# Optimization experiments

Measured on AMD Instinct MI355X. Metric: run time of the kernel, lower is better.

The kernel has to match this reference:

```python
import jax, jax.numpy as jnp
import numpy as np
from jax.scipy.special import erf

# synthetic covalent radii table (original imports `covalent_radii`, e.g. from ase)
COV_RADII = jnp.asarray(0.3 + 0.02 * np.arange(100), dtype=jnp.float32)

B_MOL = 1024   # molecules per batch
N_ATOM = 128   # atoms per molecule (equal-sized ragged batch, atoms sorted by molecule)
N_ELEM = 10


def setup_inputs() -> dict:
    key = jax.random.key(0)
    ks = jax.random.split(key, 6)
    N = B_MOL * N_ATOM
    return {
        "eneg": jax.random.normal(ks[0], (N, 1), jnp.float32),
        "positions": jax.random.normal(ks[1], (N, 3), jnp.float32) * 3.0,
        "node_attrs": jax.random.uniform(ks[2], (N, N_ELEM), jnp.float32),
        "hardness": jax.random.uniform(ks[3], (N_ELEM,), jnp.float32),
        "total_charge": jax.random.normal(ks[4], (B_MOL,), jnp.float32),
        "batch": jnp.repeat(jnp.arange(B_MOL), N_ATOM),          # sorted molecule ids
        "atomic_numbers": jax.random.randint(ks[5], (N,), 1, 90),
    }


def reference(eneg, positions, node_attrs, hardness, total_charge, batch, atomic_numbers):
    # atoms are sorted by molecule with equal molecule sizes, so the ragged
    # python loop of the original collapses to a batched [B, n, ...] computation.
    B = total_charge.shape[0]
    N = positions.shape[0]
    n = N // B
    sqrt_pi = jnp.sqrt(jnp.asarray(np.pi, jnp.float32))
    sqrt_2 = jnp.sqrt(jnp.asarray(2.0, jnp.float32))

    pos = positions.reshape(B, n, 3)
    Z = atomic_numbers.reshape(B, n)
    atom_idx = jnp.argmax(node_attrs, axis=1).reshape(B, n)

    r = COV_RADII[Z]                                     # [B, n]
    diag_vals = hardness[atom_idx] + 1.0 / (sqrt_pi * r)  # [B, n]
    sigma = jnp.square(r)                                # [B, n]
    gamma = jnp.sqrt(sigma[:, :, None] + sigma[:, None, :])  # [B, n, n]

    diff = pos[:, :, None, :] - pos[:, None, :, :]       # [B, n, n, 3]
    sq = jnp.sum(diff * diff, axis=-1)                   # [B, n, n]
    eye = jnp.eye(n, dtype=bool)
    dist = jnp.sqrt(jnp.where(eye, 1.0, sq))             # safe diag (overwritten below)

    A = erf(dist / (sqrt_2 * gamma)) / dist              # [B, n, n]
    A = jnp.where(eye, diag_vals[:, :, None], A)         # scatter hardness diagonal

    # augment with charge-conservation row/column of ones (corner = 1)
    A = jnp.concatenate([A, jnp.ones((B, n, 1), A.dtype)], axis=2)
    A = jnp.concatenate([A, jnp.ones((B, 1, n + 1), A.dtype)], axis=1)

    b = jnp.concatenate([-eneg.reshape(B, n, 1),
                         total_charge.reshape(B, 1, 1)], axis=1)  # [B, n+1, 1]

    x = jnp.linalg.solve(A, b)                           # batched small solves
    return x[:, :n, 0].reshape(-1)                       # partial charges, [N]
```

## Files before the change

kernel.cpp:

```cpp
#include <hip/hip_runtime.h>
#include <math.h>

#define NMOL  1024
#define N     128
#define NELEM 10
#define BLOCK 256
#define PW    8
#define NPAN  16
#define PSTR  12
#define USTR  132

typedef __attribute__((ext_vector_type(4))) float f4;


__global__ __launch_bounds__(BLOCK, 2) void ceq_solve_kernel(
    const float* __restrict__ eneg,
    const float* __restrict__ positions,
    const float* __restrict__ node_attrs,
    const float* __restrict__ hardness,
    const float* __restrict__ total_charge,
    const int*   __restrict__ atomic_numbers,
    float* __restrict__ out)
{
    __shared__ __align__(16) float P[2][2][N * PSTR];
    __shared__ __align__(16) float Up[2][PW * USTR];
    __shared__ __align__(16) float Ublk[2][NPAN][PW][PW];
    __shared__ float Dinv[2][PW], Dd[2][PW];
    __shared__ float rhsY[2][N], rhsZ[2][N];
    __shared__ float sxY[2][N], sxZ[2][N];
    __shared__ float px[2][N], py[2][N], pz[2][N], sg[2][N], dgv[2][N];
    __shared__ float lamS[2];

    const int tid  = threadIdx.x;
    const int lane = tid & 63;
    const int g    = tid >> 7;
    const int gt   = tid & 127;
    const int wv   = (tid >> 6) & 1;
    const int r0   = 2 * lane;
    const int r1   = r0 + 1;
    const int mol  = 2 * blockIdx.x + g;
    const int base = mol * N;

    {
        const int i = gt;
        const int Z = atomic_numbers[base + i];
        const float rad = 0.3f + 0.02f * (float)Z;
        sg[g][i] = 2.0f * rad * rad;
        const float* na = node_attrs + (size_t)(base + i) * NELEM;
        float best = na[0]; int bi = 0;
        #pragma unroll
        for (int e = 1; e < NELEM; ++e) {
            float v = na[e];
            if (v > best) { best = v; bi = e; }
        }
        dgv[g][i] = hardness[bi] + 0.5641895835477563f / rad;
        const float* p = positions + (size_t)(base + i) * 3;
        px[g][i] = p[0]; py[g][i] = p[1]; pz[g][i] = p[2];
        rhsY[g][i] = -eneg[base + i];
        rhsZ[g][i] = 1.0f;
    }
    __syncthreads();

    f4 Ar0[16], Ar1[16];
    {
        const float x0 = px[g][r0], y0 = py[g][r0], z0 = pz[g][r0];
        const float s0 = sg[g][r0], d0 = dgv[g][r0];
        const float x1 = px[g][r1], y1 = py[g][r1], z1 = pz[g][r1];
        const float s1 = sg[g][r1], d1 = dgv[g][r1];
        #pragma unroll
        for (int c = 0; c < 16; ++c) {
            const int jb = 16 * (c >> 1) + 8 * wv + 4 * (c & 1);
            f4 v0, v1;
            #pragma unroll
            for (int e = 0; e < 4; ++e) {
                const int j = jb + e;
                float a0, a1;
                if (j == r0) a0 = d0;
                else {
                    const float dx = x0 - px[g][j], dy = y0 - py[g][j], dz = z0 - pz[g][j];
                    const float d2 = dx * dx + dy * dy + dz * dz;
                    const float rd = rsqrtf(d2);
                    const float rg = rsqrtf(s0 + sg[g][j]);
                    a0 = erff(d2 * rd * rg) * rd;
                }
                if (j == r1) a1 = d1;
                else {
                    const float dx = x1 - px[g][j], dy = y1 - py[g][j], dz = z1 - pz[g][j];
                    const float d2 = dx * dx + dy * dy + dz * dz;
                    const float rd = rsqrtf(d2);
                    const float rg = rsqrtf(s1 + sg[g][j]);
                    a1 = erff(d2 * rd * rg) * rd;
                }
                ((float*)&v0)[e] = a0;
                ((float*)&v1)[e] = a1;
            }
            Ar0[c] = v0;
            Ar1[c] = v1;
        }
    }

    for (int p = 0; p < NPAN; ++p) {
        const int k0 = PW * p;
        const int q  = (p >> 1) & 7;
        float* Pc = &P[g][p & 1][0];

        if (p > 0) {
            const int pm = p - 1;
            float* Pp = &P[g][pm & 1][0];
            if (lane >= 4 * pm && lane < 4 * pm + 4) {
                const int u0 = r0 - PW * pm, u1 = u0 + 1;
                #pragma unroll
                for (int c = 0; c < 16; ++c) {
                    const int t  = 2 * (c >> 1) + wv;
                    const int gc = 4 * (c >> 1) + 2 * wv + (c & 1);
                    if (t > pm) {
                        Ar0[c] = *(const f4*)&Up[g][u0 * USTR + 4 * gc];
                        Ar1[c] = *(const f4*)&Up[g][u1 * USTR + 4 * gc];
                    }
                }
            }
            const bool hasmat = (14 + wv) > pm;
            if (hasmat && lane >= 4 * pm + 4) {
                float lA0[PW], lA1[PW];
                {
                    f4 a = *(const f4*)&Pp[r0 * PSTR], b = *(const f4*)&Pp[r0 * PSTR + 4];
                    lA0[0]=a.x; lA0[1]=a.y; lA0[2]=a.z; lA0[3]=a.w;
                    lA0[4]=b.x; lA0[5]=b.y; lA0[6]=b.z; lA0[7]=b.w;
                    f4 c2 = *(const f4*)&Pp[r1 * PSTR], d2 = *(const f4*)&Pp[r1 * PSTR + 4];
                    lA1[0]=c2.x; lA1[1]=c2.y; lA1[2]=c2.z; lA1[3]=c2.w;
                    lA1[4]=d2.x; lA1[5]=d2.y; lA1[6]=d2.z; lA1[7]=d2.w;
                }
                #pragma unroll
                for (int c = 0; c < 16; ++c) {
                    const int t  = 2 * (c >> 1) + wv;
                    const int gc = 4 * (c >> 1) + 2 * wv + (c & 1);
                    if (t > pm) {
                        f4 acc0 = Ar0[c], acc1 = Ar1[c];
                        #pragma unroll
                        for (int u = 0; u < PW; ++u) {
                            const f4 uv = *(const f4*)&Up[g][u * USTR + 4 * gc];
                            acc0 -= uv * lA0[u];
                            acc1 -= uv * lA1[u];
                        }
                        Ar0[c] = acc0; Ar1[c] = acc1;
                    }
                }
            }
        }
        if (wv == (p & 1) && lane >= 4 * p) {
            f4 a00, a01, a10, a11;
            switch (q) {
                case 0:  a00 = Ar0[0];  a01 = Ar0[1];  a10 = Ar1[0];  a11 = Ar1[1];  break;
                case 1:  a00 = Ar0[2];  a01 = Ar0[3];  a10 = Ar1[2];  a11 = Ar1[3];  break;
                case 2:  a00 = Ar0[4];  a01 = Ar0[5];  a10 = Ar1[4];  a11 = Ar1[5];  break;
                case 3:  a00 = Ar0[6];  a01 = Ar0[7];  a10 = Ar1[6];  a11 = Ar1[7];  break;
                case 4:  a00 = Ar0[8];  a01 = Ar0[9];  a10 = Ar1[8];  a11 = Ar1[9];  break;
                case 5:  a00 = Ar0[10]; a01 = Ar0[11]; a10 = Ar1[10]; a11 = Ar1[11]; break;
                case 6:  a00 = Ar0[12]; a01 = Ar0[13]; a10 = Ar1[12]; a11 = Ar1[13]; break;
                default: a00 = Ar0[14]; a01 = Ar0[15]; a10 = Ar1[14]; a11 = Ar1[15]; break;
            }
            if (lane >= 4 * p + 4) {
                *(f4*)&Pc[r0 * PSTR + 0] = a00; *(f4*)&Pc[r0 * PSTR + 4] = a01;
                *(f4*)&Pc[r1 * PSTR + 0] = a10; *(f4*)&Pc[r1 * PSTR + 4] = a11;
            } else {
                float u0[PW] = { a00.x, a00.y, a00.z, a00.w, a01.x, a01.y, a01.z, a01.w };
                float u1[PW] = { a10.x, a10.y, a10.z, a10.w, a11.x, a11.y, a11.z, a11.w };
                float ry0 = rhsY[g][r0], rz0 = rhsZ[g][r0];
                float ry1 = rhsY[g][r1], rz1 = rhsZ[g][r1];
                const int rl = lane - 4 * p;
                #pragma unroll
                for (int kk = 0; kk < PW; ++kk) {
                    const int src = 4 * p + (kk >> 1);
                    float pr[PW];
                    #pragma unroll
                    for (int j = kk; j < PW; ++j)
                        pr[j] = __shfl((kk & 1) ? u1[j] : u0[j], src);
                    const float cY = __shfl((kk & 1) ? ry1 : ry0, src);
                    const float cZ = __shfl((kk & 1) ? rz1 : rz0, src);
                    const float dinv = 1.0f / pr[kk];
                    if (2 * rl > kk) {
                        const float m = u0[kk] * dinv; u0[kk] = m;
                        #pragma unroll
                        for (int j = kk + 1; j < PW; ++j) u0[j] -= m * pr[j];
                        ry0 -= m * cY; rz0 -= m * cZ;
                    }
                    if (2 * rl + 1 > kk) {
                        const float m = u1[kk] * dinv; u1[kk] = m;
                        #pragma unroll
                        for (int j = kk + 1; j < PW; ++j) u1[j] -= m * pr[j];
                        ry1 -= m * cY; rz1 -= m * cZ;
                    }
                    if (rl == (kk >> 1)) { Dinv[g][kk] = dinv; Dd[g][kk] = pr[kk]; }
                }
                f4 w0 = { u0[0], u0[1], u0[2], u0[3] }, w1 = { u0[4], u0[5], u0[6], u0[7] };
                *(f4*)&Ublk[g][p][2 * rl][0] = w0; *(f4*)&Ublk[g][p][2 * rl][4] = w1;
                f4 w2 = { u1[0], u1[1], u1[2], u1[3] }, w3 = { u1[4], u1[5], u1[6], u1[7] };
                *(f4*)&Ublk[g][p][2 * rl + 1][0] = w2; *(f4*)&Ublk[g][p][2 * rl + 1][4] = w3;
                rhsY[g][r0] = ry0; rhsZ[g][r0] = rz0;
                rhsY[g][r1] = ry1; rhsZ[g][r1] = rz1;
            }
        }
        __syncthreads();

        const int nb = (N - PW) - k0;
        if (gt < nb) {
            const int i = k0 + PW + gt;
            f4 a = *(const f4*)&Pc[i * PSTR], b = *(const f4*)&Pc[i * PSTR + 4];
            float av[PW] = { a.x, a.y, a.z, a.w, b.x, b.y, b.z, b.w };
            float m[PW];
            #pragma unroll
            for (int j = 0; j < PW; ++j) {
                float acc = av[j];
                #pragma unroll
                for (int t = 0; t < j; ++t) acc -= m[t] * Ublk[g][p][t][j];
                m[j] = acc * Dinv[g][j];
            }
            f4 ma = { m[0], m[1], m[2], m[3] }, mb = { m[4], m[5], m[6], m[7] };
            *(f4*)&Pc[i * PSTR]     = ma;
            *(f4*)&Pc[i * PSTR + 4] = mb;
            #pragma unroll
            for (int u = 0; u < PW; ++u) Up[g][u * USTR + i] = m[u] * Dd[g][u];
            float ry = rhsY[g][i], rz = rhsZ[g][i];
            #pragma unroll
            for (int t = 0; t < PW; ++t) {
                ry -= m[t] * rhsY[g][k0 + t];
                rz -= m[t] * rhsZ[g][k0 + t];
            }
            rhsY[g][i] = ry; rhsZ[g][i] = rz;
        }
        __syncthreads();
    }

    for (int pb = NPAN - 1; pb >= 0; --pb) {
        const int k0 = PW * pb;
        if (tid < 4) {
            const int gg = tid >> 1;
            float* rhs = (tid & 1) ? rhsZ[gg] : rhsY[gg];
            float* sx  = (tid & 1) ? sxZ[gg]  : sxY[gg];
            float x[PW];
            #pragma unroll
            for (int kk = PW - 1; kk >= 0; --kk) {
                float acc = rhs[k0 + kk];
                #pragma unroll
                for (int jj = kk + 1; jj < PW; ++jj) acc -= Ublk[gg][pb][kk][jj] * x[jj];
                x[kk] = acc / Ublk[gg][pb][kk][kk];
                sx[k0 + kk] = x[kk];
            }
        }
        __syncthreads();
        if (wv == (pb & 1) && lane < 4 * pb) {
            f4 a00, a01, a10, a11;
            switch ((pb >> 1) & 7) {
                case 0:  a00 = Ar0[0];  a01 = Ar0[1];  a10 = Ar1[0];  a11 = Ar1[1];  break;
                case 1:  a00 = Ar0[2];  a01 = Ar0[3];  a10 = Ar1[2];  a11 = Ar1[3];  break;
                case 2:  a00 = Ar0[4];  a01 = Ar0[5];  a10 = Ar1[4];  a11 = Ar1[5];  break;
                case 3:  a00 = Ar0[6];  a01 = Ar0[7];  a10 = Ar1[6];  a11 = Ar1[7];  break;
                case 4:  a00 = Ar0[8];  a01 = Ar0[9];  a10 = Ar1[8];  a11 = Ar1[9];  break;
                case 5:  a00 = Ar0[10]; a01 = Ar0[11]; a10 = Ar1[10]; a11 = Ar1[11]; break;
                case 6:  a00 = Ar0[12]; a01 = Ar0[13]; a10 = Ar1[12]; a11 = Ar1[13]; break;
                default: a00 = Ar0[14]; a01 = Ar0[15]; a10 = Ar1[14]; a11 = Ar1[15]; break;
            }
            float yy0 = rhsY[g][r0], yy1 = rhsY[g][r1];
            float zz0 = rhsZ[g][r0], zz1 = rhsZ[g][r1];
            yy0 -= a00.x*sxY[g][k0]   + a00.y*sxY[g][k0+1] + a00.z*sxY[g][k0+2] + a00.w*sxY[g][k0+3]
                 + a01.x*sxY[g][k0+4] + a01.y*sxY[g][k0+5] + a01.z*sxY[g][k0+6] + a01.w*sxY[g][k0+7];
            yy1 -= a10.x*sxY[g][k0]   + a10.y*sxY[g][k0+1] + a10.z*sxY[g][k0+2] + a10.w*sxY[g][k0+3]
                 + a11.x*sxY[g][k0+4] + a11.y*sxY[g][k0+5] + a11.z*sxY[g][k0+6] + a11.w*sxY[g][k0+7];
            zz0 -= a00.x*sxZ[g][k0]   + a00.y*sxZ[g][k0+1] + a00.z*sxZ[g][k0+2] + a00.w*sxZ[g][k0+3]
                 + a01.x*sxZ[g][k0+4] + a01.y*sxZ[g][k0+5] + a01.z*sxZ[g][k0+6] + a01.w*sxZ[g][k0+7];
            zz1 -= a10.x*sxZ[g][k0]   + a10.y*sxZ[g][k0+1] + a10.z*sxZ[g][k0+2] + a10.w*sxZ[g][k0+3]
                 + a11.x*sxZ[g][k0+4] + a11.y*sxZ[g][k0+5] + a11.z*sxZ[g][k0+6] + a11.w*sxZ[g][k0+7];
            rhsY[g][r0] = yy0; rhsY[g][r1] = yy1;
            rhsZ[g][r0] = zz0; rhsZ[g][r1] = zz1;
        }
        __syncthreads();
    }

    if (wv == 0) {
        float vY = sxY[g][lane] + sxY[g][lane + 64];
        float vZ = sxZ[g][lane] + sxZ[g][lane + 64];
        #pragma unroll
        for (int off = 32; off; off >>= 1) {
            vY += __shfl_xor(vY, off);
            vZ += __shfl_xor(vZ, off);
        }
        if (lane == 0) lamS[g] = (vY - total_charge[mol]) / (vZ - 1.0f);
    }
    __syncthreads();
    out[base + gt] = sxY[g][gt] - lamS[g] * sxZ[g][gt];
}

extern "C" void kernel_launch(void* const* d_in, const int* in_sizes, int n_in,
                              void* d_out, int out_size, void* d_ws, size_t ws_size,
                              hipStream_t stream) {
    const float* eneg           = (const float*)d_in[0];
    const float* positions      = (const float*)d_in[1];
    const float* node_attrs     = (const float*)d_in[2];
    const float* hardness       = (const float*)d_in[3];
    const float* total_charge   = (const float*)d_in[4];
    const int*   atomic_numbers = (const int*)d_in[6];
    float* out = (float*)d_out;

    ceq_solve_kernel<<<NMOL / 2, BLOCK, 0, stream>>>(
        eneg, positions, node_attrs, hardness, total_charge, atomic_numbers, out);
}
```

Before: 194.2 us.

## Fuse back-substitution diagonal solve into update wave, halving barriers per panel

Back-substitution used to run in two phases per panel: four threads solved the 8x8 diagonal block serially, then a barrier, then one wave applied that block's contribution to earlier rows. Now one wave applies the previous panel's update and solves the current diagonal block in parallel across lanes, passing each solved value by shuffle. That needs only one barrier per panel, and multiplying by stored reciprocal pivots removes the divides. Per-panel inverse diagonals are now kept in shared memory for this, at the cost of a little more shared memory and more register and shuffle work in the active wave.

New measurement: 291.3 us. +50.0%, slower.

```diff
diff --git a/kernel.cpp b/kernel.cpp
--- a/kernel.cpp
+++ b/kernel.cpp
@@ -25,7 +25,8 @@
     __shared__ __align__(16) float P[2][2][N * PSTR];
     __shared__ __align__(16) float Up[2][PW * USTR];
     __shared__ __align__(16) float Ublk[2][NPAN][PW][PW];
-    __shared__ float Dinv[2][PW], Dd[2][PW];
+    __shared__ float DinvAll[2][NPAN][PW];
+    __shared__ float Dd[2][PW];
     __shared__ float rhsY[2][N], rhsZ[2][N];
     __shared__ float sxY[2][N], sxZ[2][N];
     __shared__ float px[2][N], py[2][N], pz[2][N], sg[2][N], dgv[2][N];
@@ -190,7 +191,7 @@
                         for (int j = kk + 1; j < PW; ++j) u1[j] -= m * pr[j];
                         ry1 -= m * cY; rz1 -= m * cZ;
                     }
-                    if (rl == (kk >> 1)) { Dinv[g][kk] = dinv; Dd[g][kk] = pr[kk]; }
+                    if (rl == (kk >> 1)) { DinvAll[g][p][kk] = dinv; Dd[g][kk] = pr[kk]; }
                 }
                 f4 w0 = { u0[0], u0[1], u0[2], u0[3] }, w1 = { u0[4], u0[5], u0[6], u0[7] };
                 *(f4*)&Ublk[g][p][2 * rl][0] = w0; *(f4*)&Ublk[g][p][2 * rl][4] = w1;
@@ -213,7 +214,7 @@
                 float acc = av[j];
                 #pragma unroll
                 for (int t = 0; t < j; ++t) acc -= m[t] * Ublk[g][p][t][j];
-                m[j] = acc * Dinv[g][j];
+                m[j] = acc * DinvAll[g][p][j];
             }
             f4 ma = { m[0], m[1], m[2], m[3] }, mb = { m[4], m[5], m[6], m[7] };
             *(f4*)&Pc[i * PSTR]     = ma;
@@ -233,45 +234,58 @@
 
     for (int pb = NPAN - 1; pb >= 0; --pb) {
         const int k0 = PW * pb;
-        if (tid < 4) {
-            const int gg = tid >> 1;
-            float* rhs = (tid & 1) ? rhsZ[gg] : rhsY[gg];
-            float* sx  = (tid & 1) ? sxZ[gg]  : sxY[gg];
-            float x[PW];
-            #pragma unroll
-            for (int kk = PW - 1; kk >= 0; --kk) {
-                float acc = rhs[k0 + kk];
-                #pragma unroll
-                for (int jj = kk + 1; jj < PW; ++jj) acc -= Ublk[gg][pb][kk][jj] * x[jj];
-                x[kk] = acc / Ublk[gg][pb][kk][kk];
-                sx[k0 + kk] = x[kk];
-            }
-        }
-        __syncthreads();
-        if (wv == (pb & 1) && lane < 4 * pb) {
-            f4 a00, a01, a10, a11;
-            switch ((pb >> 1) & 7) {
-                case 0:  a00 = Ar0[0];  a01 = Ar0[1];  a10 = Ar1[0];  a11 = Ar1[1];  break;
-                case 1:  a00 = Ar0[2];  a01 = Ar0[3];  a10 = Ar1[2];  a11 = Ar1[3];  break;
-                case 2:  a00 = Ar0[4];  a01 = Ar0[5];  a10 = Ar1[4];  a11 = Ar1[5];  break;
-                case 3:  a00 = Ar0[6];  a01 = Ar0[7];  a10 = Ar1[6];  a11 = Ar1[7];  break;
-                case 4:  a00 = Ar0[8];  a01 = Ar0[9];  a10 = Ar1[8];  a11 = Ar1[9];  break;
-                case 5:  a00 = Ar0[10]; a01 = Ar0[11]; a10 = Ar1[10]; a11 = Ar1[11]; break;
-                case 6:  a00 = Ar0[12]; a01 = Ar0[13]; a10 = Ar1[12]; a11 = Ar1[13]; break;
-                default: a00 = Ar0[14]; a01 = Ar0[15]; a10 = Ar1[14]; a11 = Ar1[15]; break;
-            }
+        if (wv == ((pb + 1) & 1) && lane < 4 * pb + 4) {
             float yy0 = rhsY[g][r0], yy1 = rhsY[g][r1];
             float zz0 = rhsZ[g][r0], zz1 = rhsZ[g][r1];
-            yy0 -= a00.x*sxY[g][k0]   + a00.y*sxY[g][k0+1] + a00.z*sxY[g][k0+2] + a00.w*sxY[g][k0+3]
-                 + a01.x*sxY[g][k0+4] + a01.y*sxY[g][k0+5] + a01.z*sxY[g][k0+6] + a01.w*sxY[g][k0+7];
-            yy1 -= a10.x*sxY[g][k0]   + a10.y*sxY[g][k0+1] + a10.z*sxY[g][k0+2] + a10.w*sxY[g][k0+3]
-                 + a11.x*sxY[g][k0+4] + a11.y*sxY[g][k0+5] + a11.z*sxY[g][k0+6] + a11.w*sxY[g][k0+7];
-            zz0 -= a00.x*sxZ[g][k0]   + a00.y*sxZ[g][k0+1] + a00.z*sxZ[g][k0+2] + a00.w*sxZ[g][k0+3]
-                 + a01.x*sxZ[g][k0+4] + a01.y*sxZ[g][k0+5] + a01.z*sxZ[g][k0+6] + a01.w*sxZ[g][k0+7];
-            zz1 -= a10.x*sxZ[g][k0]   + a10.y*sxZ[g][k0+1] + a10.z*sxZ[g][k0+2] + a10.w*sxZ[g][k0+3]
-                 + a11.x*sxZ[g][k0+4] + a11.y*sxZ[g][k0+5] + a11.z*sxZ[g][k0+6] + a11.w*sxZ[g][k0+7];
-            rhsY[g][r0] = yy0; rhsY[g][r1] = yy1;
-            rhsZ[g][r0] = zz0; rhsZ[g][r1] = zz1;
+            if (pb < NPAN - 1) {
+                f4 a00, a01, a10, a11;
+                switch ((pb + 1) >> 1) {
+                    case 0:  a00 = Ar0[0];  a01 = Ar0[1];  a10 = Ar1[0];  a11 = Ar1[1];  break;
+                    case 1:  a00 = Ar0[2];  a01 = Ar0[3];  a10 = Ar1[2];  a11 = Ar1[3];  break;
+                    case 2:  a00 = Ar0[4];  a01 = Ar0[5];  a10 = Ar1[4];  a11 = Ar1[5];  break;
+                    case 3:  a00 = Ar0[6];  a01 = Ar0[7];  a10 = Ar1[6];  a11 = Ar1[7];  break;
+                    case 4:  a00 = Ar0[8];  a01 = Ar0[9];  a10 = Ar1[8];  a11 = Ar1[9];  break;
+                    case 5:  a00 = Ar0[10]; a01 = Ar0[11]; a10 = Ar1[10]; a11 = Ar1[11]; break;
+                    case 6:  a00 = Ar0[12]; a01 = Ar0[13]; a10 = Ar1[12]; a11 = Ar1[13]; break;
+                    default: a00 = Ar0[14]; a01 = Ar0[15]; a10 = Ar1[14]; a11 = Ar1[15]; break;
+                }
+                const int ku = k0 + PW;
+                yy0 -= a00.x*sxY[g][ku]   + a00.y*sxY[g][ku+1] + a00.z*sxY[g][ku+2] + a00.w*sxY[g][ku+3]
+                     + a01.x*sxY[g][ku+4] + a01.y*sxY[g][ku+5] + a01.z*sxY[g][ku+6] + a01.w*sxY[g][ku+7];
+                yy1 -= a10.x*sxY[g][ku]   + a10.y*sxY[g][ku+1] + a10.z*sxY[g][ku+2] + a10.w*sxY[g][ku+3]
+                     + a11.x*sxY[g][ku+4] + a11.y*sxY[g][ku+5] + a11.z*sxY[g][ku+6] + a11.w*sxY[g][ku+7];
+                zz0 -= a00.x*sxZ[g][ku]   + a00.y*sxZ[g][ku+1] + a00.z*sxZ[g][ku+2] + a00.w*sxZ[g][ku+3]
+                     + a01.x*sxZ[g][ku+4] + a01.y*sxZ[g][ku+5] + a01.z*sxZ[g][ku+6] + a01.w*sxZ[g][ku+7];
+                zz1 -= a10.x*sxZ[g][ku]   + a10.y*sxZ[g][ku+1] + a10.z*sxZ[g][ku+2] + a10.w*sxZ[g][ku+3]
+                     + a11.x*sxZ[g][ku+4] + a11.y*sxZ[g][ku+5] + a11.z*sxZ[g][ku+6] + a11.w*sxZ[g][ku+7];
+            }
+            if (lane >= 4 * pb) {
+                const int u0 = r0 - k0;
+                #pragma unroll
+                for (int kk = PW - 1; kk >= 0; --kk) {
+                    const int src = 4 * pb + (kk >> 1);
+                    const float di = DinvAll[g][pb][kk];
+                    const float cy = ((kk & 1) ? yy1 : yy0) * di;
+                    const float cz = ((kk & 1) ? zz1 : zz0) * di;
+                    const float xky = __shfl(cy, src);
+                    const float xkz = __shfl(cz, src);
+                    if (lane == src) {
+                        if (kk & 1) { sxY[g][r1] = xky; sxZ[g][r1] = xkz; }
+                        else        { sxY[g][r0] = xky; sxZ[g][r0] = xkz; }
+                    }
+                    if (u0 < kk) {
+                        const float u = Ublk[g][pb][u0][kk];
+                        yy0 -= u * xky; zz0 -= u * xkz;
+                    }
+                    if (u0 + 1 < kk) {
+                        const float u = Ublk[g][pb][u0 + 1][kk];
+                        yy1 -= u * xky; zz1 -= u * xkz;
+                    }
+                }
+            } else {
+                rhsY[g][r0] = yy0; rhsY[g][r1] = yy1;
+                rhsZ[g][r0] = zz0; rhsZ[g][r1] = zz1;
+            }
         }
         __syncthreads();
     }
```
